# Performance work log

Measured on AMD Instinct MI355X. Metric: run time of the kernel, lower is better.

The kernel has to match this reference:

```python
import jax, jax.numpy as jnp
import numpy as np

B, L, C, D, H, NB, K = 8, 1024, 4, 64, 8, 2, 16  # batch, seq, conds, dim, heads, blocks, rbf centers

def _ln(x, s, b):
    m = x.mean(-1, keepdims=True)
    v = x.var(-1, keepdims=True)
    return (x - m) / jnp.sqrt(v + 1e-6) * s + b

def setup_inputs() -> dict:
    key = jax.random.key(0)
    ks = jax.random.split(key, 24)
    rn = lambda i, shape, sc=0.02: jax.random.normal(ks[i], shape, jnp.float32) * sc
    inp = {}
    inp['z'] = jax.random.normal(ks[0], (B, L), jnp.float32)
    inp['conditionals'] = jax.random.normal(ks[1], (C,), jnp.float32)
    inp['s'] = jnp.sort(jax.random.uniform(ks[2], (L,), jnp.float32))
    inp['embed'] = rn(3, (L, 2 * D - (C + 1)))  # positional id embedding table
    # input MLP([4D, D]) with gelu
    inp['Win1'] = rn(4, (2 * D, 4 * D)); inp['bin1'] = jnp.zeros((4 * D,), jnp.float32)
    inp['Win2'] = rn(5, (4 * D, D));     inp['bin2'] = jnp.zeros((D,), jnp.float32)
    # per-block (leading dim NB) transformer params
    inp['ln1_s'] = jnp.ones((NB, D), jnp.float32); inp['ln1_b'] = jnp.zeros((NB, D), jnp.float32)
    inp['ln2_s'] = jnp.ones((NB, D), jnp.float32); inp['ln2_b'] = jnp.zeros((NB, D), jnp.float32)
    inp['Wq'] = rn(6, (NB, D, 2 * D)); inp['bq'] = jnp.zeros((NB, 2 * D), jnp.float32)
    inp['Wk'] = rn(7, (NB, D, 2 * D)); inp['bk'] = jnp.zeros((NB, 2 * D), jnp.float32)
    inp['Wv'] = rn(8, (NB, D, 2 * D)); inp['bv'] = jnp.zeros((NB, 2 * D), jnp.float32)
    inp['Wo'] = rn(9, (NB, 2 * D, D)); inp['bo'] = jnp.zeros((NB, D), jnp.float32)
    # RBF-network attention bias: features exp(-(d-c)^2/(2w^2)) -> linear to H heads
    inp['rbf_c'] = jnp.tile(jnp.linspace(-1.0, 1.0, K, dtype=jnp.float32)[None], (NB, 1))
    inp['rbf_logw'] = jnp.full((NB, K), -1.0, jnp.float32)
    inp['rbf_w'] = rn(10, (NB, K, H), 0.1); inp['rbf_b'] = jnp.zeros((NB, H), jnp.float32)
    # FFN MLP([4D, D])
    inp['W1'] = rn(11, (NB, D, 4 * D)); inp['b1'] = jnp.zeros((NB, 4 * D), jnp.float32)
    inp['W2'] = rn(12, (NB, 4 * D, D)); inp['b2'] = jnp.zeros((NB, D), jnp.float32)
    # head MLP([4D, D, 1])
    inp['Wh1'] = rn(13, (D, 4 * D)); inp['bh1'] = jnp.zeros((4 * D,), jnp.float32)
    inp['Wh2'] = rn(14, (4 * D, D)); inp['bh2'] = jnp.zeros((D,), jnp.float32)
    inp['Wh3'] = rn(15, (D, 1));     inp['bh3'] = jnp.zeros((1,), jnp.float32)
    return inp

def reference(z, conditionals, s, embed, Win1, bin1, Win2, bin2,
              ln1_s, ln1_b, ln2_s, ln2_b, Wq, bq, Wk, bk, Wv, bv, Wo, bo,
              rbf_c, rbf_logw, rbf_w, rbf_b, W1, b1, W2, b2,
              Wh1, bh1, Wh2, bh2, Wh3, bh3):
    Bn, Ln = z.shape
    Cn = conditionals.shape[0]
    Hn = rbf_w.shape[-1]
    dh = Wq.shape[-1] // Hn
    scale = 1.0 / jnp.sqrt(jnp.float32(dh))
    # cond_as_feats: [z, broadcast conditionals] -> (B, L, C+1); prepend ids embedding -> (B, L, 2D)
    feats = jnp.concatenate([
        jnp.broadcast_to(embed[None], (Bn,) + embed.shape),
        z[..., None],
        jnp.broadcast_to(conditionals[None, None, :], (Bn, Ln, Cn)),
    ], axis=-1)
    x = jax.nn.gelu(feats @ Win1 + bin1) @ Win2 + bin2  # (B, L, D)
    dist = s[:, None] - s[None, :]  # (L, L) pairwise query-key coordinate diff (same per batch)
    for i in range(Wq.shape[0]):
        h = _ln(x, ln1_s[i], ln1_b[i])
        q = (h @ Wq[i] + bq[i]).reshape(Bn, Ln, Hn, dh)
        k = (h @ Wk[i] + bk[i]).reshape(Bn, Ln, Hn, dh)
        v = (h @ Wv[i] + bv[i]).reshape(Bn, Ln, Hn, dh)
        scores = jnp.einsum('bqhd,bkhd->bhqk', q, k) * scale
        # RBF-network bias on pairwise distances, per head
        phi = jnp.exp(-(dist[..., None] - rbf_c[i]) ** 2 / (2.0 * jnp.exp(rbf_logw[i]) ** 2))  # (L, L, K)
        bias = jnp.einsum('qkf,fh->hqk', phi, rbf_w[i]) + rbf_b[i][:, None, None]  # (H, L, L)
        a = jax.nn.softmax(scores + bias[None], axis=-1)
        o = jnp.einsum('bhqk,bkhd->bqhd', a, v).reshape(Bn, Ln, Hn * dh)
        x = x + o @ Wo[i] + bo[i]
        h2 = _ln(x, ln2_s[i], ln2_b[i])
        x = x + jax.nn.gelu(h2 @ W1[i] + b1[i]) @ W2[i] + b2[i]
    hh = jax.nn.gelu(x @ Wh1 + bh1)
    hh = jax.nn.gelu(hh @ Wh2 + bh2)
    return hh @ Wh3 + bh3  # f_hat: (B, L, 1)
```

## Files before the change

kernel.cpp:

```cpp
#include <hip/hip_runtime.h>
#include <hip/hip_bf16.h>

#define BB   8
#define LL   1024
#define DD   64
#define D2   128
#define D4   256
#define HH   8
#define DH   16

typedef __attribute__((ext_vector_type(8))) short short8;
typedef __attribute__((ext_vector_type(4))) float floatx4;

#define LOG2E 1.4426950408889634f
#define QK_SEED -66.54214054f

#define OB_QUAR 1048576
#define L_QUAR  65536

#define OFF_WIN1   0
#define OFF_WIN2   65536
#define OFF_LAY0   98304
#define LAY_STRIDE 131072
#define OFF_WQ     0
#define OFF_WK     16384
#define OFF_WV     32768
#define OFF_WO     49152
#define OFF_W1     65536
#define OFF_W2     98304
#define OFF_WH1    360448
#define OFF_WH2    393216

__device__ __forceinline__ float gelu_tanh(float u) {
  float y = 0.7978845608028654f * (u + 0.044715f * u * u * u);
  return __fdividef(u, 1.0f + __expf(-2.0f * y));
}

__device__ __forceinline__ float wave_reduce_sum(float v) {
#pragma unroll
  for (int m = 32; m >= 1; m >>= 1) v += __shfl_xor(v, m, 64);
  return v;
}

__device__ __forceinline__ unsigned short f2bf(float x) {
  unsigned u = __float_as_uint(x);
  u += 0x7fffu + ((u >> 16) & 1u);
  return (unsigned short)(u >> 16);
}

__device__ __forceinline__ float bf2f(unsigned short x) {
  return __uint_as_float(((unsigned)x) << 16);
}

__device__ __forceinline__ void split_bf(float v, unsigned short& hi,
                                         unsigned short& lo) {
  hi = f2bf(v);
  lo = f2bf(v - bf2f(hi));
}

__device__ __forceinline__ unsigned pack_bf2(float a, float b) {
  unsigned ua = __float_as_uint(a) + 0x8000u;
  unsigned ub = __float_as_uint(b) + 0x8000u;
  return __builtin_amdgcn_perm(ub, ua, 0x07060302u);
}

__device__ __forceinline__ int frag_off(int k, int n, int K) {
  return (n >> 4) * (K * 16) + ((k >> 5) << 9) + (((k >> 3) & 3) << 7) +
         ((n & 15) << 3) + (k & 7);
}

template <int K, int KP>
__device__ __forceinline__ floatx4 mfma_tile(
    const unsigned short* Ah, const unsigned short* Al,
    const unsigned short* __restrict__ Bf, const unsigned short* __restrict__ Bfl,
    int lane, int lq, int quad, floatx4 C) {
  floatx4 C1 = {0.0f, 0.0f, 0.0f, 0.0f};
  floatx4 C2 = {0.0f, 0.0f, 0.0f, 0.0f};
#pragma unroll
  for (int kk = 0; kk < K; kk += 32) {
    short8 ah = *(const short8*)(Ah + lq * KP + kk + quad * 8);
    short8 al = *(const short8*)(Al + lq * KP + kk + quad * 8);
    short8 bh = *(const short8*)(Bf + (kk >> 5) * 512 + lane * 8);
    short8 bl = *(const short8*)(Bfl + (kk >> 5) * 512 + lane * 8);
    C  = __builtin_amdgcn_mfma_f32_16x16x32_bf16(ah, bh, C, 0, 0, 0);
    C1 = __builtin_amdgcn_mfma_f32_16x16x32_bf16(al, bh, C1, 0, 0, 0);
    C2 = __builtin_amdgcn_mfma_f32_16x16x32_bf16(ah, bl, C2, 0, 0, 0);
  }
#pragma unroll
  for (int r = 0; r < 4; ++r) C[r] += C1[r] + C2[r];
  return C;
}

struct PrepArgs {
  const float* src[16];
  int Kd[16], Nd[16], dst[16], elems[16];
};

__global__ __launch_bounds__(256) void k_prep_bias(
    PrepArgs a, unsigned short* __restrict__ arena,
    const float* __restrict__ s, const float* __restrict__ rbf_c,
    const float* __restrict__ rbf_logw, const float* __restrict__ rbf_w,
    const float* __restrict__ rbf_b, unsigned short* __restrict__ biasT) {
  int bid = blockIdx.x, t = threadIdx.x;
  if (bid < 2048) {
    int mid = bid >> 7;
    int e = (bid & 127) * 256 + t;
    int KN = a.elems[mid];
    if (e >= KN) return;
    int K = a.Kd[mid], N = a.Nd[mid];
    int n = e / K, k = e - n * K;
    float wv = a.src[mid][k * N + n];
    unsigned short hi, lo;
    split_bf(wv, hi, lo);
    int fo = frag_off(k, n, K);
    arena[a.dst[mid] + fo] = hi;
    arena[a.dst[mid] + KN + fo] = lo;
    return;
  }
  __shared__ float cs[16], iw[16];
  int rem = bid - 2048;
  int lay = rem >> 12;
  if (t < 16) {
    cs[t] = rbf_c[lay * 16 + t];
    iw[t] = 0.5f * __expf(-2.0f * rbf_logw[lay * 16 + t]);
  }
  __syncthreads();
  int id = (rem & 4095) * 256 + t;
  int q = id >> 10, k = id & 1023;
  float dd = s[q] - s[k];
  float acc[8];
#pragma unroll
  for (int h = 0; h < 8; ++h) acc[h] = rbf_b[lay * 8 + h];
#pragma unroll 1
  for (int f = 0; f < 16; ++f) {
    float e = dd - cs[f];
    float ph = __expf(-e * e * iw[f]);
#pragma unroll
    for (int h = 0; h < 8; ++h)
      acc[h] = fmaf(ph, rbf_w[lay * 128 + f * 8 + h], acc[h]);
  }
  unsigned short* bT = biasT + (size_t)lay * 8 * 1024 * 1024;
#pragma unroll
  for (int h = 0; h < 8; ++h)
    bT[(size_t)(h * 1024 + q) * 1024 + k] = f2bf(acc[h] * LOG2E);
}

__device__ __forceinline__ void qkv_tail(
    const float* xl, unsigned short* Sh, unsigned short* Sl,
    const unsigned short* __restrict__ arena, int lay,
    const float* __restrict__ ln_s, const float* __restrict__ ln_b,
    const float* __restrict__ bq, const float* __restrict__ bk,
    const float* __restrict__ bv, unsigned short* __restrict__ qo,
    unsigned short* __restrict__ ko, unsigned short* __restrict__ voT,
    int tok0, int t) {
  int w = t >> 6, lane = t & 63;
  int lq = lane & 15, quad = lane >> 4;
  float ss = ln_s[lay * 64 + lane], sb = ln_b[lay * 64 + lane];
#pragma unroll
  for (int tk = 0; tk < 2; ++tk) {
    int tok = w * 2 + tk;
    float v = xl[tok * 64 + lane];
    float s1 = v, s2 = v * v;
#pragma unroll
    for (int m = 32; m >= 1; m >>= 1) {
      s1 += __shfl_xor(s1, m, 64);
      s2 += __shfl_xor(s2, m, 64);
    }
    float mean = s1 * 0.015625f;
    float var = fmaf(-mean, mean, s2 * 0.015625f);
    float hv = (v - mean) * rsqrtf(var + 1e-6f) * ss + sb;
    unsigned short hi, lo;
    split_bf(hv, hi, lo);
    Sh[tok * 72 + lane] = hi;
    Sl[tok * 72 + lane] = lo;
  }
  __syncthreads();
  int b = tok0 >> 10, l0 = tok0 & 1023;
  int tl = w;
#pragma unroll 1
  for (int mat = 0; mat < 3; ++mat) {
    const unsigned short* Bh =
        arena + OFF_LAY0 + lay * LAY_STRIDE + mat * 16384;
    const unsigned short* Bl = Bh + 8192;
    const float* bias = (mat == 0 ? bq : mat == 1 ? bk : bv) + lay * 128;
    int n = tl * 16 + lq;
    float bb = bias[n];
    floatx4 C = {bb, bb, bb, bb};
    C = mfma_tile<64, 72>(Sh, Sl, Bh + tl * 16 * 64, Bl + tl * 16 * 64,
                          lane, lq, quad, C);
    if (mat < 2) {
      unsigned short* outp = (mat == 0 ? qo : ko);
      size_t basea = ((size_t)(b * 8 + tl) * 1024 + l0 + quad * 4) * 16 + lq;
#pragma unroll
      for (int r = 0; r < 4; ++r)
        outp[basea + (size_t)r * 16] = f2bf(C[r]);
    } else {
      size_t basev = ((size_t)(b * 8 + tl) * 16 + lq) * 1024 + l0 + quad * 4;
#pragma unroll
      for (int r = 0; r < 4; ++r)
        voT[basev + r] = f2bf(C[r]);
    }
  }
}

__global__ __launch_bounds__(512, 4) void k_in_qkv(
    const float* __restrict__ embed, const float* __restrict__ z,
    const float* __restrict__ cond, const unsigned short* __restrict__ arena,
    const float* __restrict__ bin1, const float* __restrict__ bin2,
    float* __restrict__ x, const float* __restrict__ ln1_s,
    const float* __restrict__ ln1_b, const float* __restrict__ bq,
    const float* __restrict__ bk, const float* __restrict__ bv,
    unsigned short* __restrict__ qo, unsigned short* __restrict__ ko,
    unsigned short* __restrict__ voT) {
  __shared__ __align__(16) unsigned short Ah[16 * 136], Al[16 * 136];
  __shared__ __align__(16) unsigned short Hh[16 * 264], Hl[16 * 264];
  __shared__ __align__(16) unsigned short Sh[16 * 72], Sl[16 * 72];
  __shared__ float xl[16 * 64];
  __shared__ __align__(16) float red[4 * 64 * 4];
  int t = threadIdx.x, w = t >> 6, lane = t & 63;
  int lq = lane & 15, quad = lane >> 4;
  int tok0 = blockIdx.x * 16;
  for (int idx = t; idx < 2048; idx += 512) {
    int tok = idx >> 7, dim = idx & 127;
    int bl = tok0 + tok, l = bl & (LL - 1);
    float v;
    if (dim < 123) v = embed[l * 123 + dim];
    else if (dim == 123) v = z[bl];
    else v = cond[dim - 124];
    unsigned short hi, lo;
    split_bf(v, hi, lo);
    Ah[tok * 136 + dim] = hi;
    Al[tok * 136 + dim] = lo;
  }
  __syncthreads();
  const unsigned short* B1h = arena + OFF_WIN1;
  const unsigned short* B1l = B1h + 32768;
#pragma unroll
  for (int j = 0; j < 2; ++j) {
    int tl = w * 2 + j, n = tl * 16 + lq;
    float bb = bin1[n];
    floatx4 C = {bb, bb, bb, bb};
    C = mfma_tile<128, 136>(Ah, Al, B1h + tl * 16 * 128, B1l + tl * 16 * 128,
                            lane, lq, quad, C);
#pragma unroll
    for (int r = 0; r < 4; ++r) {
      float g = gelu_tanh(C[r]);
      unsigned short hi, lo;
      split_bf(g, hi, lo);
      Hh[(quad * 4 + r) * 264 + n] = hi;
      Hl[(quad * 4 + r) * 264 + n] = lo;
    }
  }
  __syncthreads();
  {
    const unsigned short* B2h = arena + OFF_WIN2;
    const unsigned short* B2l = B2h + 16384;
    int tile = w & 3, kh = w >> 2, koff = kh * 128;
    int n = tile * 16 + lq;
    floatx4 C = {0.0f, 0.0f, 0.0f, 0.0f};
    if (kh == 0) {
      float bb = bin2[n];
      C[0] = bb; C[1] = bb; C[2] = bb; C[3] = bb;
    }
    C = mfma_tile<128, 264>(Hh + koff, Hl + koff,
                            B2h + tile * 16 * 256 + (koff >> 5) * 512,
                            B2l + tile * 16 * 256 + (koff >> 5) * 512,
                            lane, lq, quad, C);
    if (kh) *(floatx4*)&red[(tile * 64 + lane) * 4] = C;
    __syncthreads();
    if (!kh) {
      floatx4 Cp = *(const floatx4*)&red[(tile * 64 + lane) * 4];
#pragma unroll
      for (int r = 0; r < 4; ++r) {
        int m = quad * 4 + r;
        float cv = C[r] + Cp[r];
        x[(size_t)(tok0 + m) * 64 + n] = cv;
        xl[m * 64 + n] = cv;
      }
    }
  }
  __syncthreads();
  qkv_tail(xl, Sh, Sl, arena, 0, ln1_s, ln1_b, bq, bk, bv,
           qo, ko, voT, tok0, t);
}

__global__ __launch_bounds__(256) void k_attn(
    const unsigned short* __restrict__ qg, const unsigned short* __restrict__ kg,
    const unsigned short* __restrict__ vgT, const unsigned short* __restrict__ biasT,
    float* __restrict__ og, float* __restrict__ lsum) {
  __shared__ __align__(16) unsigned short Kl[64 * 40];
  __shared__ __align__(16) unsigned short VT[16 * 72];
  __shared__ __align__(16) unsigned short Pl[4][16 * 72];
  __shared__ __align__(16) unsigned short Bch[64 * 72];
  int t = threadIdx.x, w = t >> 6, lane = t & 63;
  int lq = lane & 15, quad = lane >> 4;
  int bid = blockIdx.x;
  int quarter = bid >> 10;
  int rem = bid & 1023;
  int b = rem >> 7, h = (rem >> 4) & 7, qblk = rem & 15;
  int q0w = qblk * 64 + w * 16;
  int kbase = quarter * 256;
  size_t bh = (size_t)(b * 8 + h) * 1024;
  size_t bh16 = (size_t)(b * 8 + h) * 16;

  ((uint4*)Kl)[t] = uint4{0, 0, 0, 0};
  if (t < 64) ((uint4*)Kl)[256 + t] = uint4{0, 0, 0, 0};

  short8 Qb = {};
  if (quad < 2)
    Qb = *(const short8*)(qg + (bh + q0w + lq) * 16 + quad * 8);

  float l = 0.0f;
  floatx4 O = {0.0f, 0.0f, 0.0f, 0.0f};

  int key = t >> 2, dp = (t & 3) * 4;
  int drow = t >> 4, vcol = (t & 15) * 4;
  int qrow = t >> 2, bcol = (t & 3) * 16;
  const unsigned short* kgp = kg + (bh + kbase + key) * 16 + dp;
  const unsigned short* vgp = vgT + (bh16 + drow) * 1024 + kbase + vcol;
  const unsigned short* bgp =
      biasT + ((size_t)(h * 1024 + qblk * 64 + qrow)) * 1024 + kbase + bcol;

  uint2 kpre = *(const uint2*)(kgp);
  uint2 vpre = *(const uint2*)(vgp);
  uint4 bpre0 = *(const uint4*)(bgp);
  uint4 bpre1 = *(const uint4*)(bgp + 8);

#pragma unroll 1
  for (int kc = 0; kc < 256; kc += 64) {
    __syncthreads();
    *(uint2*)(Kl + key * 40 + dp) = kpre;
    *(uint2*)(VT + drow * 72 + vcol) = vpre;
    *(uint4*)(Bch + qrow * 72 + bcol) = bpre0;
    *(uint4*)(Bch + qrow * 72 + bcol + 8) = bpre1;
    __syncthreads();
    if (kc + 64 < 256) {
      kpre = *(const uint2*)(kgp + (size_t)(kc + 64) * 16);
      vpre = *(const uint2*)(vgp + (kc + 64));
      bpre0 = *(const uint4*)(bgp + (kc + 64));
      bpre1 = *(const uint4*)(bgp + (kc + 64) + 8);
    }
    float psum = 0.0f;
    unsigned short* pw = &Pl[w][lq * 72];
#pragma unroll
    for (int tile = 0; tile < 4; ++tile) {
      short8 A = *(const short8*)(Kl + (tile * 16 + lq) * 40 + quad * 8);
      floatx4 c = {QK_SEED, QK_SEED, QK_SEED, QK_SEED};
      c = __builtin_amdgcn_mfma_f32_16x16x32_bf16(A, Qb, c, 0, 0, 0);
      ushort4 bb = *(const ushort4*)(Bch + (w * 16 + lq) * 72 +
                                     tile * 16 + quad * 4);
      float p0 = exp2f(fmaf(c[0], 0.25f * LOG2E, bf2f(bb.x)));
      float p1 = exp2f(fmaf(c[1], 0.25f * LOG2E, bf2f(bb.y)));
      float p2 = exp2f(fmaf(c[2], 0.25f * LOG2E, bf2f(bb.z)));
      float p3 = exp2f(fmaf(c[3], 0.25f * LOG2E, bf2f(bb.w)));
      psum += (p0 + p1) + (p2 + p3);
      uint2 pk;
      pk.x = pack_bf2(p0, p1);
      pk.y = pack_bf2(p2, p3);
      *(uint2*)(pw + tile * 16 + quad * 4) = pk;
    }
    psum += __shfl_xor(psum, 16, 64);
    psum += __shfl_xor(psum, 32, 64);
    l += psum;
    asm volatile("s_waitcnt lgkmcnt(0)" ::: "memory");
#pragma unroll
    for (int i = 0; i < 2; ++i) {
      short8 Pa = *(const short8*)(pw + i * 32 + quad * 8);
      short8 Vb = *(const short8*)(&VT[lq * 72 + i * 32 + quad * 8]);
      O = __builtin_amdgcn_mfma_f32_16x16x32_bf16(Pa, Vb, O, 0, 0, 0);
    }
  }
  float* ogh = og + (size_t)quarter * OB_QUAR;
#pragma unroll
  for (int r = 0; r < 4; ++r)
    ogh[((size_t)(b * 1024 + q0w + quad * 4 + r)) * 128 + h * 16 + lq] = O[r];
  if (quad == 0)
    lsum[(size_t)quarter * L_QUAR + (size_t)(b * 1024 + q0w + lq) * 8 + h] = l;
}

__device__ __forceinline__ void pf_body(
    const float* __restrict__ ob, const float* __restrict__ lsum,
    const unsigned short* __restrict__ arena,
    const float* __restrict__ bo, float* __restrict__ x,
    const float* __restrict__ ln_s, const float* __restrict__ ln_b,
    const float* __restrict__ b1, const float* __restrict__ b2, int lay,
    unsigned short* Ah, unsigned short* Al, unsigned short* Sh,
    unsigned short* Sl, unsigned short* Hh, unsigned short* Hl, float* xl,
    float* red, int tok0, int t, bool write_x) {
  int w = t >> 6, lane = t & 63;
  int lq = lane & 15, quad = lane >> 4;
  const unsigned short* labase = arena + OFF_LAY0 + lay * LAY_STRIDE;
  const float* ob1 = ob + OB_QUAR;
  const float* ob2 = ob + 2 * OB_QUAR;
  const float* ob3 = ob + 3 * OB_QUAR;
  {
    int idx = t * 4;
    int row = idx >> 7, col = idx & 127;
    int hh = col >> 4;
    int tok = tok0 + row;
    float lv = ((lsum[(size_t)tok * 8 + hh] +
                 lsum[L_QUAR + (size_t)tok * 8 + hh]) +
                (lsum[2 * L_QUAR + (size_t)tok * 8 + hh] +
                 lsum[3 * L_QUAR + (size_t)tok * 8 + hh]));
    float linv = 1.0f / lv;
    float4 v0 = *(const float4*)(ob + (size_t)tok * 128 + col);
    float4 v1 = *(const float4*)(ob1 + (size_t)tok * 128 + col);
    float4 v2 = *(const float4*)(ob2 + (size_t)tok * 128 + col);
    float4 v3 = *(const float4*)(ob3 + (size_t)tok * 128 + col);
    float4 v;
    v.x = ((v0.x + v1.x) + (v2.x + v3.x)) * linv;
    v.y = ((v0.y + v1.y) + (v2.y + v3.y)) * linv;
    v.z = ((v0.z + v1.z) + (v2.z + v3.z)) * linv;
    v.w = ((v0.w + v1.w) + (v2.w + v3.w)) * linv;
    unsigned short h0, e0, h1, e1, h2, e2, h3, e3;
    split_bf(v.x, h0, e0); split_bf(v.y, h1, e1);
    split_bf(v.z, h2, e2); split_bf(v.w, h3, e3);
    unsigned* ph = (unsigned*)(Ah + row * 136 + col);
    ph[0] = (unsigned)h0 | ((unsigned)h1 << 16);
    ph[1] = (unsigned)h2 | ((unsigned)h3 << 16);
    unsigned* pl = (unsigned*)(Al + row * 136 + col);
    pl[0] = (unsigned)e0 | ((unsigned)e1 << 16);
    pl[1] = (unsigned)e2 | ((unsigned)e3 << 16);
  }
  __syncthreads();
  {
    const unsigned short* Bh = labase + OFF_WO;
    const unsigned short* Bl = Bh + 8192;
    int tile = w & 3, kh = w >> 2, koff = kh * 64;
    int n = tile * 16 + lq;
    floatx4 C = {0.0f, 0.0f, 0.0f, 0.0f};
    if (kh == 0) {
      float bb = bo[lay * 64 + n];
      C[0] = bb; C[1] = bb; C[2] = bb; C[3] = bb;
    }
    C = mfma_tile<64, 136>(Ah + koff, Al + koff,
                           Bh + tile * 16 * 128 + (koff >> 5) * 512,
                           Bl + tile * 16 * 128 + (koff >> 5) * 512,
                           lane, lq, quad, C);
    if (kh) *(floatx4*)&red[(tile * 64 + lane) * 4] = C;
    __syncthreads();
    if (!kh) {
      floatx4 Cp = *(const floatx4*)&red[(tile * 64 + lane) * 4];
#pragma unroll
      for (int r = 0; r < 4; ++r) {
        int m = quad * 4 + r;
        xl[m * 64 + n] = x[(size_t)(tok0 + m) * 64 + n] + C[r] + Cp[r];
      }
    }
  }
  __syncthreads();
  {
    float ss = ln_s[lay * 64 + lane], sb = ln_b[lay * 64 + lane];
#pragma unroll
    for (int tk = 0; tk < 2; ++tk) {
      int tok = w * 2 + tk;
      float v = xl[tok * 64 + lane];
      float s1 = v, s2 = v * v;
#pragma unroll
      for (int m = 32; m >= 1; m >>= 1) {
        s1 += __shfl_xor(s1, m, 64);
        s2 += __shfl_xor(s2, m, 64);
      }
      float mean = s1 * 0.015625f;
      float var = fmaf(-mean, mean, s2 * 0.015625f);
      float hv = (v - mean) * rsqrtf(var + 1e-6f) * ss + sb;
      unsigned short hi, lo;
      split_bf(hv, hi, lo);
      Sh[tok * 72 + lane] = hi;
      Sl[tok * 72 + lane] = lo;
    }
  }
  __syncthreads();
  {
    const unsigned short* Bh = labase + OFF_W1;
    const unsigned short* Bl = Bh + 16384;
#pragma unroll
    for (int j = 0; j < 2; ++j) {
      int tl = w * 2 + j, n = tl * 16 + lq;
      float bb = b1[lay * 256 + n];
      floatx4 C = {bb, bb, bb, bb};
      C = mfma_tile<64, 72>(Sh, Sl, Bh + tl * 16 * 64, Bl + tl * 16 * 64,
                            lane, lq, quad, C);
#pragma unroll
      for (int r = 0; r < 4; ++r) {
        float g = gelu_tanh(C[r]);
        unsigned short hi, lo;
        split_bf(g, hi, lo);
        Hh[(quad * 4 + r) * 264 + n] = hi;
        Hl[(quad * 4 + r) * 264 + n] = lo;
      }
    }
  }
  __syncthreads();
  {
    const unsigned short* Bh = labase + OFF_W2;
    const unsigned short* Bl = Bh + 16384;
    int tile = w & 3, kh = w >> 2, koff = kh * 128;
    int n = tile * 16 + lq;
    floatx4 C = {0.0f, 0.0f, 0.0f, 0.0f};
    if (kh == 0) {
      float bb = b2[lay * 64 + n];
      C[0] = bb; C[1] = bb; C[2] = bb; C[3] = bb;
    }
    C = mfma_tile<128, 264>(Hh + koff, Hl + koff,
                            Bh + tile * 16 * 256 + (koff >> 5) * 512,
                            Bl + tile * 16 * 256 + (koff >> 5) * 512,
                            lane, lq, quad, C);
    if (kh) *(floatx4*)&red[(tile * 64 + lane) * 4] = C;
    __syncthreads();
    if (!kh) {
      floatx4 Cp = *(const floatx4*)&red[(tile * 64 + lane) * 4];
#pragma unroll
      for (int r = 0; r < 4; ++r) {
        int m = quad * 4 + r;
        float xv = xl[m * 64 + n] + C[r] + Cp[r];
        xl[m * 64 + n] = xv;
        if (write_x) x[(size_t)(tok0 + m) * 64 + n] = xv;
      }
    }
  }
  __syncthreads();
}

__global__ __launch_bounds__(512, 4) void k_pf_qkv(
    const float* __restrict__ ob, const float* __restrict__ lsum,
    const unsigned short* __restrict__ arena,
    const float* __restrict__ bo, float* __restrict__ x,
    const float* __restrict__ ln2_s, const float* __restrict__ ln2_b,
    const float* __restrict__ b1, const float* __restrict__ b2, int lay,
    const float* __restrict__ ln1_s, const float* __restrict__ ln1_b,
    const float* __restrict__ bq, const float* __restrict__ bk,
    const float* __restrict__ bv, unsigned short* __restrict__ qo,
    unsigned short* __restrict__ ko, unsigned short* __restrict__ voT) {
  __shared__ __align__(16) unsigned short Ah[16 * 136], Al[16 * 136];
  __shared__ __align__(16) unsigned short Sh[16 * 72], Sl[16 * 72];
  __shared__ __align__(16) unsigned short Hh[16 * 264], Hl[16 * 264];
  __shared__ float xl[16 * 64];
  __shared__ __align__(16) float red[4 * 64 * 4];
  int t = threadIdx.x;
  int tok0 = blockIdx.x * 16;
  pf_body(ob, lsum, arena, bo, x, ln2_s, ln2_b, b1, b2, lay,
          Ah, Al, Sh, Sl, Hh, Hl, xl, red, tok0, t, true);
  qkv_tail(xl, Sh, Sl, arena, lay + 1, ln1_s, ln1_b, bq, bk, bv,
           qo, ko, voT, tok0, t);
}

__global__ __launch_bounds__(512, 4) void k_pf_head(
    const float* __restrict__ ob, const float* __restrict__ lsum,
    const unsigned short* __restrict__ arena,
    const float* __restrict__ bo, float* __restrict__ x,
    const float* __restrict__ ln2_s, const float* __restrict__ ln2_b,
    const float* __restrict__ b1, const float* __restrict__ b2, int lay,
    const float* __restrict__ bh1, const float* __restrict__ bh2,
    const float* __restrict__ Wh3, const float* __restrict__ bh3,
    float* __restrict__ out) {
  __shared__ __align__(16) unsigned short Ah[16 * 136], Al[16 * 136];
  __shared__ __align__(16) unsigned short Sh[16 * 72], Sl[16 * 72];
  __shared__ __align__(16) unsigned short Hh[16 * 264], Hl[16 * 264];
  __shared__ float xl[16 * 64];
  __shared__ __align__(16) float red[4 * 64 * 4];
  int t = threadIdx.x, w = t >> 6, lane = t & 63;
  int lq = lane & 15, quad = lane >> 4;
  int tok0 = blockIdx.x * 16;
  pf_body(ob, lsum, arena, bo, x, ln2_s, ln2_b, b1, b2, lay,
          Ah, Al, Sh, Sl, Hh, Hl, xl, red, tok0, t, false);
#pragma unroll
  for (int tk = 0; tk < 2; ++tk) {
    int tok = w * 2 + tk;
    unsigned short hi, lo;
    split_bf(xl[tok * 64 + lane], hi, lo);
    Sh[tok * 72 + lane] = hi;
    Sl[tok * 72 + lane] = lo;
  }
  __syncthreads();
  {
    const unsigned short* Bh = arena + OFF_WH1;
    const unsigned short* Bl = Bh + 16384;
#pragma unroll
    for (int j = 0; j < 2; ++j) {
      int tl = w * 2 + j, n = tl * 16 + lq;
      float bb = bh1[n];
      floatx4 C = {bb, bb, bb, bb};
      C = mfma_tile<64, 72>(Sh, Sl, Bh + tl * 16 * 64, Bl + tl * 16 * 64,
                            lane, lq, quad, C);
#pragma unroll
      for (int r = 0; r < 4; ++r) {
        float g = gelu_tanh(C[r]);
        unsigned short hi, lo;
        split_bf(g, hi, lo);
        Hh[(quad * 4 + r) * 264 + n] = hi;
        Hl[(quad * 4 + r) * 264 + n] = lo;
      }
    }
  }
  __syncthreads();
  {
    const unsigned short* Bh = arena + OFF_WH2;
    const unsigned short* Bl = Bh + 16384;
    int tile = w & 3, kh = w >> 2, koff = kh * 128;
    int n = tile * 16 + lq;
    floatx4 C = {0.0f, 0.0f, 0.0f, 0.0f};
    if (kh == 0) {
      float bb = bh2[n];
      C[0] = bb; C[1] = bb; C[2] = bb; C[3] = bb;
    }
    C = mfma_tile<128, 264>(Hh + koff, Hl + koff,
                            Bh + tile * 16 * 256 + (koff >> 5) * 512,
                            Bl + tile * 16 * 256 + (koff >> 5) * 512,
                            lane, lq, quad, C);
    if (kh) *(floatx4*)&red[(tile * 64 + lane) * 4] = C;
    __syncthreads();
    if (!kh) {
      floatx4 Cp = *(const floatx4*)&red[(tile * 64 + lane) * 4];
#pragma unroll
      for (int r = 0; r < 4; ++r)
        xl[(quad * 4 + r) * 64 + n] = gelu_tanh(C[r] + Cp[r]);
    }
  }
  __syncthreads();
  float wv3 = Wh3[lane];
#pragma unroll
  for (int tk = 0; tk < 2; ++tk) {
    int tok = w * 2 + tk;
    float v = xl[tok * 64 + lane] * wv3;
    float sum = wave_reduce_sum(v);
    if (lane == 0) out[tok0 + tok] = sum + bh3[0];
  }
}

extern "C" void kernel_launch(void* const* d_in, const int* in_sizes, int n_in,
                              void* d_out, int out_size, void* d_ws, size_t ws_size,
                              hipStream_t stream) {
  const float* z      = (const float*)d_in[0];
  const float* cond   = (const float*)d_in[1];
  const float* s      = (const float*)d_in[2];
  const float* embed  = (const float*)d_in[3];
  const float* Win1   = (const float*)d_in[4];
  const float* bin1   = (const float*)d_in[5];
  const float* Win2   = (const float*)d_in[6];
  const float* bin2   = (const float*)d_in[7];
  const float* ln1_s  = (const float*)d_in[8];
  const float* ln1_b  = (const float*)d_in[9];
  const float* ln2_s  = (const float*)d_in[10];
  const float* ln2_b  = (const float*)d_in[11];
  const float* Wq     = (const float*)d_in[12];
  const float* bq     = (const float*)d_in[13];
  const float* Wk     = (const float*)d_in[14];
  const float* bk     = (const float*)d_in[15];
  const float* Wv     = (const float*)d_in[16];
  const float* bv     = (const float*)d_in[17];
  const float* Wo     = (const float*)d_in[18];
  const float* bo     = (const float*)d_in[19];
  const float* rbf_c  = (const float*)d_in[20];
  const float* rbf_lw = (const float*)d_in[21];
  const float* rbf_w  = (const float*)d_in[22];
  const float* rbf_b  = (const float*)d_in[23];
  const float* W1     = (const float*)d_in[24];
  const float* b1     = (const float*)d_in[25];
  const float* W2     = (const float*)d_in[26];
  const float* b2     = (const float*)d_in[27];
  const float* Wh1    = (const float*)d_in[28];
  const float* bh1    = (const float*)d_in[29];
  const float* Wh2    = (const float*)d_in[30];
  const float* bh2    = (const float*)d_in[31];
  const float* Wh3    = (const float*)d_in[32];
  const float* bh3    = (const float*)d_in[33];

  char* base = (char*)d_ws;
  float*          x     = (float*)(base);
  unsigned short* qb    = (unsigned short*)(base + (2u << 20));
  unsigned short* kb    = (unsigned short*)(base + (4u << 20));
  unsigned short* vbT   = (unsigned short*)(base + (6u << 20));
  float*          ob    = (float*)(base + (8u << 20));
  float*          lsum  = (float*)(base + (24u << 20));
  unsigned short* biasT = (unsigned short*)(base + (25u << 20));
  unsigned short* arena = (unsigned short*)(base + (57u << 20));

  PrepArgs pa;
  auto set = [&](int i, const float* sp, int K, int N, int dst) {
    pa.src[i] = sp; pa.Kd[i] = K; pa.Nd[i] = N; pa.dst[i] = dst;
    pa.elems[i] = K * N;
  };
  set(0, Win1, 128, 256, OFF_WIN1);
  set(1, Win2, 256, 64, OFF_WIN2);
  for (int lay = 0; lay < 2; ++lay) {
    int lb = OFF_LAY0 + lay * LAY_STRIDE;
    set(2 + lay * 6, Wq + lay * 8192, 64, 128, lb + OFF_WQ);
    set(3 + lay * 6, Wk + lay * 8192, 64, 128, lb + OFF_WK);
    set(4 + lay * 6, Wv + lay * 8192, 64, 128, lb + OFF_WV);
    set(5 + lay * 6, Wo + lay * 8192, 128, 64, lb + OFF_WO);
    set(6 + lay * 6, W1 + lay * 16384, 64, 256, lb + OFF_W1);
    set(7 + lay * 6, W2 + lay * 16384, 256, 64, lb + OFF_W2);
  }
  set(14, Wh1, 64, 256, OFF_WH1);
  set(15, Wh2, 256, 64, OFF_WH2);

  k_prep_bias<<<2048 + 8192, 256, 0, stream>>>(pa, arena, s, rbf_c, rbf_lw,
                                               rbf_w, rbf_b, biasT);
  k_in_qkv<<<512, 512, 0, stream>>>(embed, z, cond, arena, bin1, bin2, x,
                                    ln1_s, ln1_b, bq, bk, bv, qb, kb, vbT);
  k_attn<<<4096, 256, 0, stream>>>(qb, kb, vbT, biasT, ob, lsum);
  k_pf_qkv<<<512, 512, 0, stream>>>(ob, lsum, arena, bo, x, ln2_s, ln2_b,
                                    b1, b2, 0, ln1_s, ln1_b, bq, bk, bv,
                                    qb, kb, vbT);
  k_attn<<<4096, 256, 0, stream>>>(qb, kb, vbT,
                                   biasT + (size_t)8 * 1024 * 1024, ob, lsum);
  k_pf_head<<<512, 512, 0, stream>>>(ob, lsum, arena, bo, x, ln2_s, ln2_b,
                                     b1, b2, 1, bh1, bh2, Wh3, bh3,
                                     (float*)d_out);
}
```

Before: 239.3 us.

## Process four batches per attention block to reuse the bias tile

Each attention workgroup now handles four batch elements for the same head, query block and key quarter. The bf16 bias tile is loaded from global memory once and shared across those four batches, so bias traffic drops fourfold and the grid shrinks from 4096 to 1024 blocks. In exchange each block holds four K/V tiles in LDS and four sets of accumulators in registers. That lowers occupancy and parallelism and lengthens the serial work per block.

```diff
diff --git a/kernel.cpp b/kernel.cpp
--- a/kernel.cpp
+++ b/kernel.cpp
@@ -288,94 +288,122 @@
     const unsigned short* __restrict__ qg, const unsigned short* __restrict__ kg,
     const unsigned short* __restrict__ vgT, const unsigned short* __restrict__ biasT,
     float* __restrict__ og, float* __restrict__ lsum) {
-  __shared__ __align__(16) unsigned short Kl[64 * 40];
-  __shared__ __align__(16) unsigned short VT[16 * 72];
+  __shared__ __align__(16) unsigned short Kl[4 * 64 * 40];
+  __shared__ __align__(16) unsigned short VT[4 * 16 * 72];
   __shared__ __align__(16) unsigned short Pl[4][16 * 72];
   __shared__ __align__(16) unsigned short Bch[64 * 72];
   int t = threadIdx.x, w = t >> 6, lane = t & 63;
   int lq = lane & 15, quad = lane >> 4;
   int bid = blockIdx.x;
-  int quarter = bid >> 10;
-  int rem = bid & 1023;
-  int b = rem >> 7, h = (rem >> 4) & 7, qblk = rem & 15;
+  int quarter = bid >> 8;
+  int rem = bid & 255;
+  int bg = rem >> 7;
+  int rem2 = rem & 127;
+  int h = rem2 >> 4, qblk = rem2 & 15;
   int q0w = qblk * 64 + w * 16;
   int kbase = quarter * 256;
-  size_t bh = (size_t)(b * 8 + h) * 1024;
-  size_t bh16 = (size_t)(b * 8 + h) * 16;
-
-  ((uint4*)Kl)[t] = uint4{0, 0, 0, 0};
-  if (t < 64) ((uint4*)Kl)[256 + t] = uint4{0, 0, 0, 0};
-
-  short8 Qb = {};
-  if (quad < 2)
-    Qb = *(const short8*)(qg + (bh + q0w + lq) * 16 + quad * 8);
-
-  float l = 0.0f;
-  floatx4 O = {0.0f, 0.0f, 0.0f, 0.0f};
+  int b0 = bg * 4;
+
+  for (int i = t; i < 1280; i += 256) ((uint4*)Kl)[i] = uint4{0, 0, 0, 0};
 
   int key = t >> 2, dp = (t & 3) * 4;
   int drow = t >> 4, vcol = (t & 15) * 4;
   int qrow = t >> 2, bcol = (t & 3) * 16;
-  const unsigned short* kgp = kg + (bh + kbase + key) * 16 + dp;
-  const unsigned short* vgp = vgT + (bh16 + drow) * 1024 + kbase + vcol;
+
+  short8 Qb[4];
+  floatx4 O[4];
+  float l[4];
+  const unsigned short* kgp[4];
+  const unsigned short* vgp[4];
+#pragma unroll
+  for (int i = 0; i < 4; ++i) {
+    size_t bh = (size_t)((b0 + i) * 8 + h) * 1024;
+    size_t bh16 = (size_t)((b0 + i) * 8 + h) * 16;
+    Qb[i] = short8{};
+    if (quad < 2)
+      Qb[i] = *(const short8*)(qg + (bh + q0w + lq) * 16 + quad * 8);
+    O[i] = floatx4{0.0f, 0.0f, 0.0f, 0.0f};
+    l[i] = 0.0f;
+    kgp[i] = kg + (bh + kbase + key) * 16 + dp;
+    vgp[i] = vgT + (bh16 + drow) * 1024 + kbase + vcol;
+  }
   const unsigned short* bgp =
       biasT + ((size_t)(h * 1024 + qblk * 64 + qrow)) * 1024 + kbase + bcol;
 
-  uint2 kpre = *(const uint2*)(kgp);
-  uint2 vpre = *(const uint2*)(vgp);
+  uint2 kpre[4], vpre[4];
+#pragma unroll
+  for (int i = 0; i < 4; ++i) {
+    kpre[i] = *(const uint2*)kgp[i];
+    vpre[i] = *(const uint2*)vgp[i];
+  }
   uint4 bpre0 = *(const uint4*)(bgp);
   uint4 bpre1 = *(const uint4*)(bgp + 8);
 
 #pragma unroll 1
   for (int kc = 0; kc < 256; kc += 64) {
     __syncthreads();
-    *(uint2*)(Kl + key * 40 + dp) = kpre;
-    *(uint2*)(VT + drow * 72 + vcol) = vpre;
+#pragma unroll
+    for (int i = 0; i < 4; ++i) {
+      *(uint2*)(Kl + i * 2560 + key * 40 + dp) = kpre[i];
+      *(uint2*)(VT + i * 1152 + drow * 72 + vcol) = vpre[i];
+    }
     *(uint4*)(Bch + qrow * 72 + bcol) = bpre0;
     *(uint4*)(Bch + qrow * 72 + bcol + 8) = bpre1;
     __syncthreads();
     if (kc + 64 < 256) {
-      kpre = *(const uint2*)(kgp + (size_t)(kc + 64) * 16);
-      vpre = *(const uint2*)(vgp + (kc + 64));
+#pragma unroll
+      for (int i = 0; i < 4; ++i) {
+        kpre[i] = *(const uint2*)(kgp[i] + (size_t)(kc + 64) * 16);
+        vpre[i] = *(const uint2*)(vgp[i] + (kc + 64));
+      }
       bpre0 = *(const uint4*)(bgp + (kc + 64));
       bpre1 = *(const uint4*)(bgp + (kc + 64) + 8);
     }
-    float psum = 0.0f;
     unsigned short* pw = &Pl[w][lq * 72];
 #pragma unroll
-    for (int tile = 0; tile < 4; ++tile) {
-      short8 A = *(const short8*)(Kl + (tile * 16 + lq) * 40 + quad * 8);
-      floatx4 c = {QK_SEED, QK_SEED, QK_SEED, QK_SEED};
-      c = __builtin_amdgcn_mfma_f32_16x16x32_bf16(A, Qb, c, 0, 0, 0);
-      ushort4 bb = *(const ushort4*)(Bch + (w * 16 + lq) * 72 +
-                                     tile * 16 + quad * 4);
-      float p0 = exp2f(fmaf(c[0], 0.25f * LOG2E, bf2f(bb.x)));
-      float p1 = exp2f(fmaf(c[1], 0.25f * LOG2E, bf2f(bb.y)));
-      float p2 = exp2f(fmaf(c[2], 0.25f * LOG2E, bf2f(bb.z)));
-      float p3 = exp2f(fmaf(c[3], 0.25f * LOG2E, bf2f(bb.w)));
-      psum += (p0 + p1) + (p2 + p3);
-      uint2 pk;
-      pk.x = pack_bf2(p0, p1);
-      pk.y = pack_bf2(p2, p3);
-      *(uint2*)(pw + tile * 16 + quad * 4) = pk;
-    }
-    psum += __shfl_xor(psum, 16, 64);
-    psum += __shfl_xor(psum, 32, 64);
-    l += psum;
-    asm volatile("s_waitcnt lgkmcnt(0)" ::: "memory");
-#pragma unroll
-    for (int i = 0; i < 2; ++i) {
-      short8 Pa = *(const short8*)(pw + i * 32 + quad * 8);
-      short8 Vb = *(const short8*)(&VT[lq * 72 + i * 32 + quad * 8]);
-      O = __builtin_amdgcn_mfma_f32_16x16x32_bf16(Pa, Vb, O, 0, 0, 0);
+    for (int i = 0; i < 4; ++i) {
+      float psum = 0.0f;
+#pragma unroll
+      for (int tile = 0; tile < 4; ++tile) {
+        short8 A = *(const short8*)(Kl + i * 2560 +
+                                    (tile * 16 + lq) * 40 + quad * 8);
+        floatx4 c = {QK_SEED, QK_SEED, QK_SEED, QK_SEED};
+        c = __builtin_amdgcn_mfma_f32_16x16x32_bf16(A, Qb[i], c, 0, 0, 0);
+        ushort4 bb = *(const ushort4*)(Bch + (w * 16 + lq) * 72 +
+                                       tile * 16 + quad * 4);
+        float p0 = exp2f(fmaf(c[0], 0.25f * LOG2E, bf2f(bb.x)));
+        float p1 = exp2f(fmaf(c[1], 0.25f * LOG2E, bf2f(bb.y)));
+        float p2 = exp2f(fmaf(c[2], 0.25f * LOG2E, bf2f(bb.z)));
+        float p3 = exp2f(fmaf(c[3], 0.25f * LOG2E, bf2f(bb.w)));
+        psum += (p0 + p1) + (p2 + p3);
+        uint2 pk;
+        pk.x = pack_bf2(p0, p1);
+        pk.y = pack_bf2(p2, p3);
+        *(uint2*)(pw + tile * 16 + quad * 4) = pk;
+      }
+      psum += __shfl_xor(psum, 16, 64);
+      psum += __shfl_xor(psum, 32, 64);
+      l[i] += psum;
+      asm volatile("s_waitcnt lgkmcnt(0)" ::: "memory");
+#pragma unroll
+      for (int j = 0; j < 2; ++j) {
+        short8 Pa = *(const short8*)(pw + j * 32 + quad * 8);
+        short8 Vb = *(const short8*)(&VT[i * 1152 + lq * 72 + j * 32 + quad * 8]);
+        O[i] = __builtin_amdgcn_mfma_f32_16x16x32_bf16(Pa, Vb, O[i], 0, 0, 0);
+      }
     }
   }
   float* ogh = og + (size_t)quarter * OB_QUAR;
 #pragma unroll
-  for (int r = 0; r < 4; ++r)
-    ogh[((size_t)(b * 1024 + q0w + quad * 4 + r)) * 128 + h * 16 + lq] = O[r];
-  if (quad == 0)
-    lsum[(size_t)quarter * L_QUAR + (size_t)(b * 1024 + q0w + lq) * 8 + h] = l;
+  for (int i = 0; i < 4; ++i) {
+#pragma unroll
+    for (int r = 0; r < 4; ++r)
+      ogh[((size_t)((b0 + i) * 1024 + q0w + quad * 4 + r)) * 128 +
+          h * 16 + lq] = O[i][r];
+    if (quad == 0)
+      lsum[(size_t)quarter * L_QUAR +
+           (size_t)((b0 + i) * 1024 + q0w + lq) * 8 + h] = l[i];
+  }
 }
 
 __device__ __forceinline__ void pf_body(
@@ -699,11 +727,11 @@
                                                rbf_w, rbf_b, biasT);
   k_in_qkv<<<512, 512, 0, stream>>>(embed, z, cond, arena, bin1, bin2, x,
                                     ln1_s, ln1_b, bq, bk, bv, qb, kb, vbT);
-  k_attn<<<4096, 256, 0, stream>>>(qb, kb, vbT, biasT, ob, lsum);
+  k_attn<<<1024, 256, 0, stream>>>(qb, kb, vbT, biasT, ob, lsum);
   k_pf_qkv<<<512, 512, 0, stream>>>(ob, lsum, arena, bo, x, ln2_s, ln2_b,
                                     b1, b2, 0, ln1_s, ln1_b, bq, bk, bv,
                                     qb, kb, vbT);
-  k_attn<<<4096, 256, 0, stream>>>(qb, kb, vbT,
+  k_attn<<<1024, 256, 0, stream>>>(qb, kb, vbT,
                                    biasT + (size_t)8 * 1024 * 1024, ob, lsum);
   k_pf_head<<<512, 512, 0, stream>>>(ob, lsum, arena, bo, x, ln2_s, ln2_b,
                                      b1, b2, 1, bh1, bh2, Wh3, bh3,
```

Measured after the change: 250.9 us. 1.05x slower.
